# Kernel optimization log

Hardware: AMD Instinct MI355X
Metric: run time of the kernel (lower is better)

Reference implementation:

```python
import jax, jax.numpy as jnp
import numpy as np

K = 3          # kernel_size
DIL = 2        # dilation
PAD = 2        # unfold padding
EPS = 1e-5     # InstanceNorm eps


def setup_inputs() -> dict:
    key = jax.random.key(0)
    ks = jax.random.split(key, 6)
    b, c, h, w = 8, 128, 128, 128
    c_red = c // 8                      # reduction_ratio = 8
    k2 = K * K
    x = jax.random.normal(ks[0], (b, c, h, w), dtype=jnp.float32)
    # conv1: 1x1, channels -> channels//8, no bias
    w1 = jax.random.normal(ks[1], (c_red, c), dtype=jnp.float32) * (1.0 / np.sqrt(c))
    # InstanceNorm2d affine params
    in_gamma = jnp.ones((c_red,), dtype=jnp.float32)
    in_beta = jnp.zeros((c_red,), dtype=jnp.float32)
    # conv2: 1x1, channels//8 -> k^2 * groups (groups == channels since group_channels=1)
    w2 = jax.random.normal(ks[2], (k2 * c, c_red), dtype=jnp.float32) * (1.0 / np.sqrt(c_red))
    b2 = jnp.zeros((k2 * c,), dtype=jnp.float32)
    return {"x": x, "w1": w1, "in_gamma": in_gamma, "in_beta": in_beta, "w2": w2, "b2": b2}


def reference(x, w1, in_gamma, in_beta, w2, b2):
    b, c, h, w = x.shape
    k2 = K * K
    # --- weight generation branch (stride == 1, ZeroPad2d arg is 0 -> no-op) ---
    t = jnp.einsum('oc,bchw->bohw', w1, x)                      # 1x1 conv, no bias
    mean = t.mean(axis=(2, 3), keepdims=True)                   # InstanceNorm2d (biased var)
    var = t.var(axis=(2, 3), keepdims=True)
    t = (t - mean) * jax.lax.rsqrt(var + EPS)
    t = t * in_gamma[None, :, None, None] + in_beta[None, :, None, None]
    t = jax.nn.relu(t)
    wgt = jnp.einsum('oc,bchw->bohw', w2, t) + b2[None, :, None, None]
    wgt = wgt.reshape(b, c, k2, h, w)                           # (b, groups=c, k^2, h, w)
    # --- unfold: dilated 3x3 patches, padding=2 -> same spatial size ---
    xp = jnp.pad(x, ((0, 0), (0, 0), (PAD, PAD), (PAD, PAD)))
    patches = jnp.stack(
        [xp[:, :, DIL * i:DIL * i + h, DIL * j:DIL * j + w]
         for i in range(K) for j in range(K)], axis=2)          # (b, c, k^2, h, w)
    # --- dynamic-weight multiply + reduce over kernel taps ---
    return (wgt * patches).sum(axis=2)                          # (b, c, h, w)
```

## Files before the change

### kernel.cpp

```cpp
#include <hip/hip_runtime.h>

#define BB   8
#define CC   128
#define CR   16
#define HH   128
#define WW   128
#define HWSZ 16384
#define K2   9
#define NFRAG 72

typedef _Float16 f16x8 __attribute__((ext_vector_type(8)));
typedef float    f32x4 __attribute__((ext_vector_type(4)));

#define WS_T     0
#define WS_PART  2097152
#define WS_STATS 2113536
#define WS_TN16  2113792
#define WS_AFRAG 3162368

__global__ __launch_bounds__(256) void k_conv1(const float* __restrict__ x,
                                               const float* __restrict__ w1,
                                               float* __restrict__ t,
                                               float* __restrict__ part) {
    const int tile = blockIdx.x;
    const int b    = blockIdx.y;
    const int tid  = threadIdx.x;
    const int pix  = tile * 256 + tid;

    __shared__ float w1s[CR * CC];
    for (int i = tid; i < CR * CC; i += 256) w1s[i] = w1[i];
    __syncthreads();

    const float* xb = x + (size_t)b * CC * HWSZ + pix;
    float acc[CR];
#pragma unroll
    for (int o = 0; o < CR; ++o) acc[o] = 0.f;

    for (int cin = 0; cin < CC; ++cin) {
        float xv = xb[(size_t)cin * HWSZ];
#pragma unroll
        for (int o = 0; o < CR; ++o)
            acc[o] = fmaf(w1s[o * CC + cin], xv, acc[o]);
    }

    float* tb = t + (size_t)b * CR * HWSZ + pix;
#pragma unroll
    for (int o = 0; o < CR; ++o) tb[(size_t)o * HWSZ] = acc[o];

    __shared__ float red[4][CR][2];
    const int lane = tid & 63;
    const int wv   = tid >> 6;
#pragma unroll
    for (int o = 0; o < CR; ++o) {
        float s = acc[o];
        float q = s * s;
#pragma unroll
        for (int off = 32; off > 0; off >>= 1) {
            s += __shfl_down(s, off, 64);
            q += __shfl_down(q, off, 64);
        }
        if (lane == 0) { red[wv][o][0] = s; red[wv][o][1] = q; }
    }
    __syncthreads();
    if (tid < CR) {
        const int o = tid;
        float s = red[0][o][0] + red[1][o][0] + red[2][o][0] + red[3][o][0];
        float q = red[0][o][1] + red[1][o][1] + red[2][o][1] + red[3][o][1];
        const int blk = b * 64 + tile;
        part[blk * 32 + o * 2 + 0] = s;
        part[blk * 32 + o * 2 + 1] = q;
    }
}

__global__ void k_stats(const float* __restrict__ part,
                        const float* __restrict__ gamma,
                        const float* __restrict__ beta,
                        float* __restrict__ stats) {
    const int b   = blockIdx.x >> 4;
    const int o   = blockIdx.x & 15;
    const int tle = threadIdx.x;
    float s = part[(b * 64 + tle) * 32 + o * 2 + 0];
    float q = part[(b * 64 + tle) * 32 + o * 2 + 1];
#pragma unroll
    for (int off = 32; off > 0; off >>= 1) {
        s += __shfl_down(s, off, 64);
        q += __shfl_down(q, off, 64);
    }
    if (tle == 0) {
        const float mean = s * (1.f / (float)HWSZ);
        const float var  = q * (1.f / (float)HWSZ) - mean * mean;
        const float rstd = rsqrtf(var + 1e-5f);
        const float sc   = gamma[o] * rstd;
        const float sh   = beta[o] - mean * sc;
        stats[(b * CR + o) * 2 + 0] = sc;
        stats[(b * CR + o) * 2 + 1] = sh;
    }
}

__global__ __launch_bounds__(256) void k_norm(const float* __restrict__ ws_t,
                                              const float* __restrict__ stats,
                                              f16x8* __restrict__ tn16) {
    const int p  = blockIdx.x * 256 + threadIdx.x;
    const int b  = p >> 14;
    const int pp = p & 16383;
    const float* tb = ws_t + (size_t)b * CR * HWSZ + pp;
    const float* st = stats + b * CR * 2;
    f16x8 lo, hi;
#pragma unroll
    for (int i = 0; i < 8; ++i) {
        float v0 = fmaf(tb[(size_t)i * HWSZ],       st[i * 2],       st[i * 2 + 1]);
        float v1 = fmaf(tb[(size_t)(i + 8) * HWSZ], st[(i + 8) * 2], st[(i + 8) * 2 + 1]);
        lo[i] = (_Float16)(v0 > 0.f ? v0 : 0.f);
        hi[i] = (_Float16)(v1 > 0.f ? v1 : 0.f);
    }
    tn16[(size_t)p * 2 + 0] = lo;
    tn16[(size_t)p * 2 + 1] = hi;
}

__global__ __launch_bounds__(256) void k_prep(const float* __restrict__ w2,
                                              const float* __restrict__ b2,
                                              float* __restrict__ ws) {
    const int id = blockIdx.x * 256 + threadIdx.x;
    if (id >= NFRAG * 64) return;
    const int lane = id & 63;
    const int frag = id >> 6;
    const int ct = frag / 9, k = frag - ct * 9;
    const int row = lane & 15, lg = lane >> 4;
    f16x8 v;
#pragma unroll
    for (int i = 0; i < 8; ++i) {
        const int kk = lg * 8 + i;
        float w = 0.f;
        if (kk < CR)        w = w2[(size_t)((ct * 16 + row) * K2 + k) * CR + kk];
        else if (kk == CR)  w = b2[(ct * 16 + row) * K2 + k];
        v[i] = (_Float16)w;
    }
    f16x8* dst = (f16x8*)(ws + WS_AFRAG);
    dst[frag * 64 + lane] = v;
}

__global__ __launch_bounds__(256) void k_main(const float* __restrict__ x,
                                              const float* __restrict__ ws,
                                              float* __restrict__ out) {
    const int bid = blockIdx.x;
    const int w   = (bid & 7) * 512 + (bid >> 3);
    const int y4    = w & 31;
    const int xhalf = (w >> 5) & 1;
    const int ct    = (w >> 6) & 7;
    const int b     = w >> 9;

    const int tid  = threadIdx.x;
    const int wv   = tid >> 6;
    const int lane = tid & 63;
    const int lg   = lane >> 4;
    const int ln   = lane & 15;
    const int y    = y4 * 4 + wv;

    const f16x8* afr = (const f16x8*)(ws + WS_AFRAG) + (size_t)ct * K2 * 64 + lane;
    f16x8 af[K2];
#pragma unroll
    for (int k = 0; k < K2; ++k) af[k] = afr[k * 64];

    const int crow = lg * 4;
    const int cb   = ct * 16 + crow;
    const float* xp = x   + ((size_t)b * CC + cb) * HWSZ;
    float*       op = out + ((size_t)b * CC + cb) * HWSZ;
    const f16x8* tns = (const f16x8*)(ws + WS_TN16) + ((size_t)b << 15);
    const bool yint = (y >= 2) && (y < HH - 2);
    const f32x4 zc = {0.f, 0.f, 0.f, 0.f};

#pragma unroll 1
    for (int g = 0; g < 4; ++g) {
        const int colb = xhalf * 64 + g * 16;
        const int col  = colb + ln;
        const int pix  = y * WW + col;

        f16x8 tnf = {};
        if (lg < 2) {
            tnf = tns[(size_t)pix * 2 + lg];
        } else if (lg == 2) {
            tnf[0] = (_Float16)1.f;
        }

        f32x4 acc = {0.f, 0.f, 0.f, 0.f};
        const bool xint = (colb >= 2) && (colb + 17 < WW);

        if (yint && xint) {
            const float* q0 = xp + pix;
            const float* q1 = q0 + HWSZ;
            const float* q2 = q0 + 2 * HWSZ;
            const float* q3 = q0 + 3 * HWSZ;
#pragma unroll
            for (int k = 0; k < K2; ++k) {
                const int d = ((k / 3) * 2 - 2) * WW + ((k % 3) * 2 - 2);
                const f32x4 wg = __builtin_amdgcn_mfma_f32_16x16x32_f16(af[k], tnf, zc, 0, 0, 0);
                acc[0] = fmaf(wg[0], q0[d], acc[0]);
                acc[1] = fmaf(wg[1], q1[d], acc[1]);
                acc[2] = fmaf(wg[2], q2[d], acc[2]);
                acc[3] = fmaf(wg[3], q3[d], acc[3]);
            }
        } else {
            int  xoff[3];
            bool xm[3];
#pragma unroll
            for (int j = 0; j < 3; ++j) {
                const int xx = col + (j * 2 - 2);
                xm[j]   = ((unsigned)xx < (unsigned)WW);
                xoff[j] = xx & (WW - 1);
            }
#pragma unroll
            for (int k = 0; k < K2; ++k) {
                const int yy  = y + ((k / 3) * 2 - 2);
                const int off = ((yy & (HH - 1)) << 7) + xoff[k % 3];
                const float m = (xm[k % 3] && ((unsigned)yy < (unsigned)HH)) ? 1.f : 0.f;
                const f32x4 wg = __builtin_amdgcn_mfma_f32_16x16x32_f16(af[k], tnf, zc, 0, 0, 0);
                acc[0] = fmaf(wg[0], xp[off + 0 * HWSZ] * m, acc[0]);
                acc[1] = fmaf(wg[1], xp[off + 1 * HWSZ] * m, acc[1]);
                acc[2] = fmaf(wg[2], xp[off + 2 * HWSZ] * m, acc[2]);
                acc[3] = fmaf(wg[3], xp[off + 3 * HWSZ] * m, acc[3]);
            }
        }

        float* o = op + pix;
        o[0 * HWSZ] = acc[0];
        o[1 * HWSZ] = acc[1];
        o[2 * HWSZ] = acc[2];
        o[3 * HWSZ] = acc[3];
    }
}

extern "C" void kernel_launch(void* const* d_in, const int* in_sizes, int n_in,
                              void* d_out, int out_size, void* d_ws, size_t ws_size,
                              hipStream_t stream) {
    const float* x     = (const float*)d_in[0];
    const float* w1    = (const float*)d_in[1];
    const float* gamma = (const float*)d_in[2];
    const float* beta  = (const float*)d_in[3];
    const float* w2    = (const float*)d_in[4];
    const float* b2    = (const float*)d_in[5];
    float* out = (float*)d_out;

    float* ws = (float*)d_ws;

    k_prep<<<18, 256, 0, stream>>>(w2, b2, ws);

    dim3 gA(64, 8);
    k_conv1<<<gA, 256, 0, stream>>>(x, w1, ws + WS_T, ws + WS_PART);

    k_stats<<<128, 64, 0, stream>>>(ws + WS_PART, gamma, beta, ws + WS_STATS);

    k_norm<<<512, 256, 0, stream>>>(ws + WS_T, ws + WS_STATS, (f16x8*)(ws + WS_TN16));

    k_main<<<4096, 256, 0, stream>>>(x, ws, out);
}
```

Measured before the change: 81.00 us.

## Fold prep and stats kernels into neighbors; prefetch next tn fragment in main

Weight fragment prep becomes extra blocks appended to the conv1 launch, and the per-instance stats reduction now runs redundantly inside each k_norm block through shared memory, cutting the launch count from five to three. k_main gets a launch-bounds occupancy hint and software-prefetches the next column group's normalized-activation fragment so that load overlaps the current group's compute. In exchange every norm block re-reduces 64 partials, and the prefetch adds registers.

```diff
diff --git a/kernel.cpp b/kernel.cpp
--- a/kernel.cpp
+++ b/kernel.cpp
@@ -14,17 +14,40 @@
 
 #define WS_T     0
 #define WS_PART  2097152
-#define WS_STATS 2113536
 #define WS_TN16  2113792
 #define WS_AFRAG 3162368
 
 __global__ __launch_bounds__(256) void k_conv1(const float* __restrict__ x,
                                                const float* __restrict__ w1,
-                                               float* __restrict__ t,
-                                               float* __restrict__ part) {
-    const int tile = blockIdx.x;
-    const int b    = blockIdx.y;
-    const int tid  = threadIdx.x;
+                                               const float* __restrict__ w2,
+                                               const float* __restrict__ b2,
+                                               float* __restrict__ ws) {
+    const int bid = blockIdx.x;
+    const int tid = threadIdx.x;
+
+    if (bid >= 512) {
+        const int id = (bid - 512) * 256 + tid;
+        if (id >= NFRAG * 64) return;
+        const int lane = id & 63;
+        const int frag = id >> 6;
+        const int ct = frag / 9, k = frag - ct * 9;
+        const int row = lane & 15, lg = lane >> 4;
+        f16x8 v;
+#pragma unroll
+        for (int i = 0; i < 8; ++i) {
+            const int kk = lg * 8 + i;
+            float w = 0.f;
+            if (kk < CR)        w = w2[(size_t)((ct * 16 + row) * K2 + k) * CR + kk];
+            else if (kk == CR)  w = b2[(ct * 16 + row) * K2 + k];
+            v[i] = (_Float16)w;
+        }
+        f16x8* dst = (f16x8*)(ws + WS_AFRAG);
+        dst[frag * 64 + lane] = v;
+        return;
+    }
+
+    const int tile = bid & 63;
+    const int b    = bid >> 6;
     const int pix  = tile * 256 + tid;
 
     __shared__ float w1s[CR * CC];
@@ -43,7 +66,7 @@
             acc[o] = fmaf(w1s[o * CC + cin], xv, acc[o]);
     }
 
-    float* tb = t + (size_t)b * CR * HWSZ + pix;
+    float* tb = ws + WS_T + (size_t)b * CR * HWSZ + pix;
 #pragma unroll
     for (int o = 0; o < CR; ++o) tb[(size_t)o * HWSZ] = acc[o];
 
@@ -67,49 +90,57 @@
         float s = red[0][o][0] + red[1][o][0] + red[2][o][0] + red[3][o][0];
         float q = red[0][o][1] + red[1][o][1] + red[2][o][1] + red[3][o][1];
         const int blk = b * 64 + tile;
+        float* part = ws + WS_PART;
         part[blk * 32 + o * 2 + 0] = s;
         part[blk * 32 + o * 2 + 1] = q;
     }
 }
 
-__global__ void k_stats(const float* __restrict__ part,
-                        const float* __restrict__ gamma,
-                        const float* __restrict__ beta,
-                        float* __restrict__ stats) {
-    const int b   = blockIdx.x >> 4;
-    const int o   = blockIdx.x & 15;
-    const int tle = threadIdx.x;
-    float s = part[(b * 64 + tle) * 32 + o * 2 + 0];
-    float q = part[(b * 64 + tle) * 32 + o * 2 + 1];
-#pragma unroll
-    for (int off = 32; off > 0; off >>= 1) {
-        s += __shfl_down(s, off, 64);
-        q += __shfl_down(q, off, 64);
-    }
-    if (tle == 0) {
-        const float mean = s * (1.f / (float)HWSZ);
-        const float var  = q * (1.f / (float)HWSZ) - mean * mean;
-        const float rstd = rsqrtf(var + 1e-5f);
-        const float sc   = gamma[o] * rstd;
-        const float sh   = beta[o] - mean * sc;
-        stats[(b * CR + o) * 2 + 0] = sc;
-        stats[(b * CR + o) * 2 + 1] = sh;
-    }
-}
-
 __global__ __launch_bounds__(256) void k_norm(const float* __restrict__ ws_t,
-                                              const float* __restrict__ stats,
+                                              const float* __restrict__ part,
+                                              const float* __restrict__ gamma,
+                                              const float* __restrict__ beta,
                                               f16x8* __restrict__ tn16) {
-    const int p  = blockIdx.x * 256 + threadIdx.x;
-    const int b  = p >> 14;
-    const int pp = p & 16383;
+    const int tid = threadIdx.x;
+    const int p   = blockIdx.x * 256 + tid;
+    const int b   = p >> 14;
+    const int pp  = p & 16383;
+
+    __shared__ float sts[CR][2];
+    {
+        const int o  = tid >> 4;
+        const int t4 = tid & 15;
+        float s = 0.f, q = 0.f;
+        if (o < CR) {
+#pragma unroll
+            for (int j = 0; j < 4; ++j) {
+                const int blk = b * 64 + t4 + j * 16;
+                s += part[blk * 32 + o * 2 + 0];
+                q += part[blk * 32 + o * 2 + 1];
+            }
+#pragma unroll
+            for (int off = 8; off > 0; off >>= 1) {
+                s += __shfl_down(s, off, 16);
+                q += __shfl_down(q, off, 16);
+            }
+            if (t4 == 0) {
+                const float mean = s * (1.f / (float)HWSZ);
+                const float var  = q * (1.f / (float)HWSZ) - mean * mean;
+                const float rstd = rsqrtf(var + 1e-5f);
+                const float sc   = gamma[o] * rstd;
+                sts[o][0] = sc;
+                sts[o][1] = beta[o] - mean * sc;
+            }
+        }
+    }
+    __syncthreads();
+
     const float* tb = ws_t + (size_t)b * CR * HWSZ + pp;
-    const float* st = stats + b * CR * 2;
     f16x8 lo, hi;
 #pragma unroll
     for (int i = 0; i < 8; ++i) {
-        float v0 = fmaf(tb[(size_t)i * HWSZ],       st[i * 2],       st[i * 2 + 1]);
-        float v1 = fmaf(tb[(size_t)(i + 8) * HWSZ], st[(i + 8) * 2], st[(i + 8) * 2 + 1]);
+        float v0 = fmaf(tb[(size_t)i * HWSZ],       sts[i][0],     sts[i][1]);
+        float v1 = fmaf(tb[(size_t)(i + 8) * HWSZ], sts[i + 8][0], sts[i + 8][1]);
         lo[i] = (_Float16)(v0 > 0.f ? v0 : 0.f);
         hi[i] = (_Float16)(v1 > 0.f ? v1 : 0.f);
     }
@@ -117,31 +148,9 @@
     tn16[(size_t)p * 2 + 1] = hi;
 }
 
-__global__ __launch_bounds__(256) void k_prep(const float* __restrict__ w2,
-                                              const float* __restrict__ b2,
-                                              float* __restrict__ ws) {
-    const int id = blockIdx.x * 256 + threadIdx.x;
-    if (id >= NFRAG * 64) return;
-    const int lane = id & 63;
-    const int frag = id >> 6;
-    const int ct = frag / 9, k = frag - ct * 9;
-    const int row = lane & 15, lg = lane >> 4;
-    f16x8 v;
-#pragma unroll
-    for (int i = 0; i < 8; ++i) {
-        const int kk = lg * 8 + i;
-        float w = 0.f;
-        if (kk < CR)        w = w2[(size_t)((ct * 16 + row) * K2 + k) * CR + kk];
-        else if (kk == CR)  w = b2[(ct * 16 + row) * K2 + k];
-        v[i] = (_Float16)w;
-    }
-    f16x8* dst = (f16x8*)(ws + WS_AFRAG);
-    dst[frag * 64 + lane] = v;
-}
-
-__global__ __launch_bounds__(256) void k_main(const float* __restrict__ x,
-                                              const float* __restrict__ ws,
-                                              float* __restrict__ out) {
+__global__ __launch_bounds__(256, 4) void k_main(const float* __restrict__ x,
+                                                 const float* __restrict__ ws,
+                                                 float* __restrict__ out) {
     const int bid = blockIdx.x;
     const int w   = (bid & 7) * 512 + (bid >> 3);
     const int y4    = w & 31;
@@ -169,18 +178,18 @@
     const bool yint = (y >= 2) && (y < HH - 2);
     const f32x4 zc = {0.f, 0.f, 0.f, 0.f};
 
+    f16x8 tnf = {}, tnf_nxt = {};
+    if (lg == 2) { tnf[0] = (_Float16)1.f; tnf_nxt[0] = (_Float16)1.f; }
+    if (lg < 2)  tnf = tns[(size_t)(y * WW + xhalf * 64 + ln) * 2 + lg];
+
 #pragma unroll 1
     for (int g = 0; g < 4; ++g) {
         const int colb = xhalf * 64 + g * 16;
         const int col  = colb + ln;
         const int pix  = y * WW + col;
 
-        f16x8 tnf = {};
-        if (lg < 2) {
-            tnf = tns[(size_t)pix * 2 + lg];
-        } else if (lg == 2) {
-            tnf[0] = (_Float16)1.f;
-        }
+        if (g < 3 && lg < 2)
+            tnf_nxt = tns[(size_t)(pix + 16) * 2 + lg];
 
         f32x4 acc = {0.f, 0.f, 0.f, 0.f};
         const bool xint = (colb >= 2) && (colb + 17 < WW);
@@ -226,6 +235,9 @@
         o[1 * HWSZ] = acc[1];
         o[2 * HWSZ] = acc[2];
         o[3 * HWSZ] = acc[3];
+
+        tnf = tnf_nxt;
+        if (lg == 2) tnf[0] = (_Float16)1.f;
     }
 }
 
@@ -242,14 +254,10 @@
 
     float* ws = (float*)d_ws;
 
-    k_prep<<<18, 256, 0, stream>>>(w2, b2, ws);
-
-    dim3 gA(64, 8);
-    k_conv1<<<gA, 256, 0, stream>>>(x, w1, ws + WS_T, ws + WS_PART);
-
-    k_stats<<<128, 64, 0, stream>>>(ws + WS_PART, gamma, beta, ws + WS_STATS);
-
-    k_norm<<<512, 256, 0, stream>>>(ws + WS_T, ws + WS_STATS, (f16x8*)(ws + WS_TN16));
+    k_conv1<<<530, 256, 0, stream>>>(x, w1, w2, b2, ws);
+
+    k_norm<<<512, 256, 0, stream>>>(ws + WS_T, ws + WS_PART, gamma, beta,
+                                    (f16x8*)(ws + WS_TN16));
 
     k_main<<<4096, 256, 0, stream>>>(x, ws, out);
 }
```

Result: slower. 101.9 us (+25.8%).
